# Optimization experiments

Hardware: AMD Instinct MI355X
Metric: run time of the kernel (lower is better)

Reference implementation:

```python
import jax, jax.numpy as jnp
import numpy as np

D_STATE = 8
D_CONV = 4
DT_RANK = 8
THRESHOLD = 0.5
KPOOL = 3
PAD = (KPOOL - 1) // 2
EPS = 1e-5


def _rmsnorm(x, w):
    return x * jax.lax.rsqrt(jnp.mean(x * x, axis=-1, keepdims=True) + EPS) * w


def _dw_causal_conv(x, w, b):
    # x: (L, T, C), w: (C, 1, K) depthwise causal conv along T
    xt = jnp.transpose(x, (0, 2, 1))  # (L, C, T)
    y = jax.lax.conv_general_dilated(
        xt, w, window_strides=(1,), padding=[(D_CONV - 1, 0)],
        dimension_numbers=('NCH', 'OIH', 'NCH'), feature_group_count=xt.shape[1])
    return jnp.transpose(y, (0, 2, 1)) + b


def _selective_scan(x, delta, A, B, Cm, D):
    # x, delta: (L,T,d); A: (d,n); B, Cm: (L,T,n); D: (d,)
    dA = jnp.exp(delta[..., None] * A)                        # (L,T,d,n)
    dBx = (delta * x)[..., None] * B[:, :, None, :]           # (L,T,d,n)
    def combine(a, b):
        a1, b1 = a
        a2, b2 = b
        return (a2 * a1, a2 * b1 + b2)
    _, h = jax.lax.associative_scan(combine, (dA, dBx), axis=1)
    y = jnp.einsum('ltdn,ltn->ltd', h, Cm)
    return y + x * D


def _mamba_block(x, in_proj, conv_w, conv_b, x_proj_w, dt_proj_w, dt_proj_b,
                 A_log_f, A_log_b, D_f, D_b, out_proj_w, rms_w):
    # single-depth bidirectional (bimamba-v2 style) block, expand=1, residual + RMSNorm
    res = x
    xn = _rmsnorm(x, rms_w)
    xz = xn @ in_proj                       # (L,T,2C)
    xi, z = jnp.split(xz, 2, axis=-1)
    xi = jax.nn.silu(_dw_causal_conv(xi, conv_w, conv_b))
    dbl = xi @ x_proj_w                     # (L,T,dt_rank+2*d_state)
    dt = dbl[..., :DT_RANK]
    Bm = dbl[..., DT_RANK:DT_RANK + D_STATE]
    Cm = dbl[..., DT_RANK + D_STATE:]
    delta = jax.nn.softplus(dt @ dt_proj_w + dt_proj_b)
    A_f = -jnp.exp(A_log_f)
    A_b = -jnp.exp(A_log_b)
    flip = lambda a: a[:, ::-1]
    y_f = _selective_scan(xi, delta, A_f, Bm, Cm, D_f)
    y_b = flip(_selective_scan(flip(xi), flip(delta), A_b, flip(Bm), flip(Cm), D_b))
    y = 0.5 * (y_f + y_b) * jax.nn.silu(z)  # if_devide_out -> average two directions
    return res + y @ out_proj_w


def reference(feats, in_proj, conv_w, conv_b, x_proj_w, dt_proj_w, dt_proj_b,
              A_log_f, A_log_b, D_f, D_b, out_proj_w, rms_w, mlp_w, mlp_b,
              record_len):
    N, C, H, W = feats.shape
    T = H * W
    rec = np.asarray(record_len)  # static ragged group sizes
    ends = np.cumsum(rec)
    starts = ends - rec
    masks = []
    for s0, L in zip(starts.tolist(), rec.tolist()):
        g = feats[s0:s0 + L]                       # (L,C,H,W)
        if L > 1:
            x = g.reshape(L, C, T).transpose(0, 2, 1)  # l c h w -> l (h w) c
            feat = _mamba_block(x, in_proj, conv_w, conv_b, x_proj_w, dt_proj_w,
                                dt_proj_b, A_log_f, A_log_b, D_f, D_b,
                                out_proj_w, rms_w)
            score = jax.nn.sigmoid(feat @ mlp_w + mlp_b)   # (L,T,1)
            ego = jnp.ones((1, T, 1), feats.dtype)
            bs = jnp.concatenate([ego, score[1:]], axis=0)
        else:
            bs = jnp.ones((1, T, 1), feats.dtype)
        bs = bs.transpose(0, 2, 1).reshape(L, 1, H, W)     # l (h w) c -> l c h w
        masks.append(jnp.where(bs > THRESHOLD, 1.0, 0.0).astype(feats.dtype))
    mask = jnp.concatenate(masks, axis=0)                  # (N,1,H,W)
    pooled = jax.lax.reduce_window(
        mask, -jnp.inf, jax.lax.max,
        window_dimensions=(1, 1, KPOOL, KPOOL), window_strides=(1, 1, 1, 1),
        padding=[(0, 0), (0, 0), (PAD, PAD), (PAD, PAD)])
    return pooled


def setup_inputs():
    key = jax.random.key(0)
    ks = jax.random.split(key, 8)
    C, H, W = 128, 96, 96
    record_len = np.array([2, 3, 1, 2, 4], dtype=np.int64)
    N = int(record_len.sum())
    s = 0.05
    A_log = jnp.log(jnp.broadcast_to(
        jnp.arange(1, D_STATE + 1, dtype=jnp.float32), (C, D_STATE)))
    return {
        'feats': jax.random.normal(ks[0], (N, C, H, W), jnp.float32),
        'in_proj': jax.random.normal(ks[1], (C, 2 * C), jnp.float32) * s,
        'conv_w': jax.random.normal(ks[2], (C, 1, D_CONV), jnp.float32) * s,
        'conv_b': jnp.zeros((C,), jnp.float32),
        'x_proj_w': jax.random.normal(ks[3], (C, DT_RANK + 2 * D_STATE), jnp.float32) * s,
        'dt_proj_w': jax.random.normal(ks[4], (DT_RANK, C), jnp.float32) * s,
        'dt_proj_b': jnp.full((C,), 0.1, jnp.float32),
        'A_log_f': A_log,
        'A_log_b': A_log,
        'D_f': jnp.ones((C,), jnp.float32),
        'D_b': jnp.ones((C,), jnp.float32),
        'out_proj_w': jax.random.normal(ks[5], (C, C), jnp.float32) * s,
        'rms_w': jnp.ones((C,), jnp.float32),
        'mlp_w': jax.random.normal(ks[6], (C, 1), jnp.float32) * s,
        'mlp_b': jnp.zeros((1,), jnp.float32),
        'record_len': jnp.asarray(record_len),
    }
```

## Files before the change

### kernel.cpp

```cpp
#include <hip/hip_runtime.h>
#include <cstdint>
#include <cstddef>

#define C_CH 128
#define T_TOK 9216
#define H_IMG 96
#define W_IMG 96
#define NSTATE 8

#define CHUNK 64
#define RHALO 32

#define MT 128
#define NT 128
#define KS 32

__device__ __forceinline__ float siluf_dev(float x) {
  return x / (1.0f + expf(-x));
}

__global__ __launch_bounds__(256) void k0_setup(
    const int* __restrict__ rec, int n_groups, int N,
    const float* __restrict__ out_proj_w, const float* __restrict__ mlp_w,
    const float* __restrict__ in_proj, const float* __restrict__ rms_w,
    float* __restrict__ vvec, int* __restrict__ slot, float* __restrict__ Bf)
{
  const int tid = threadIdx.x;
  if (tid == 0) {
    int f = 0, sl = 0;
    for (int g = 0; g < n_groups; ++g) {
      const int L = rec[g];
      slot[f] = -1;
      for (int i = 1; i < L; ++i) slot[f + i] = sl++;
      f += L;
    }
  }
  if (tid < C_CH) {
    float acc = 0.0f;
    for (int j = 0; j < C_CH; ++j) acc += out_proj_w[tid * C_CH + j] * mlp_w[j];
    vvec[tid] = acc;
  }
  for (int idx = tid; idx < C_CH * 256; idx += 256) {
    const int k = idx >> 8;
    Bf[idx] = in_proj[idx] * rms_w[k];
  }
}

__global__ __launch_bounds__(256, 4) void k1_gemm(
    const float* __restrict__ feats, const float* __restrict__ Bf,
    const float* __restrict__ mlp_w, const float* __restrict__ mlp_b,
    const float* __restrict__ vvec, const int* __restrict__ slot,
    float* __restrict__ xipre, float* __restrict__ wbuf,
    float* __restrict__ logit)
{
  __shared__ float Asm[KS * MT];
  __shared__ float Bsm[KS * NT];
  __shared__ float redS[256], redR[256], irS[MT];
  const int f = blockIdx.z;
  const int s = slot[f];
  if (s < 0) return;
  const int m0 = blockIdx.x * MT;
  const int nch = blockIdx.y;
  const int j0 = nch * NT;
  const int tid = threadIdx.x;
  const int tm = tid & 15;
  const int tn = tid >> 4;
  const size_t fbase = (size_t)f * C_CH * T_TOK;
  const size_t rowbase = (size_t)s * T_TOK;

  float acc[8][8];
  #pragma unroll
  for (int i = 0; i < 8; ++i)
    #pragma unroll
    for (int j = 0; j < 8; ++j) acc[i][j] = 0.0f;
  float ssum = 0.0f, rmsum = 0.0f;
  const int tokA = tid & 127;
  const int khalf = tid >> 7;

  for (int ks = 0; ks < 4; ++ks) {
    const int k0 = ks * KS;
    __syncthreads();
    #pragma unroll
    for (int i = 0; i < 4; ++i) {
      const int idx = tid + 256 * i;
      const int r = idx >> 5;
      const int q = (idx & 31) * 4;
      *(float4*)&Asm[r * MT + q] =
          *(const float4*)&feats[fbase + (size_t)(k0 + r) * T_TOK + m0 + q];
      *(float4*)&Bsm[r * NT + q] =
          *(const float4*)&Bf[(k0 + r) * 256 + j0 + q];
    }
    __syncthreads();
    #pragma unroll
    for (int kk = 0; kk < 16; ++kk) {
      const int k = khalf * 16 + kk;
      const float v = Asm[k * MT + tokA];
      ssum = fmaf(v, v, ssum);
      rmsum = fmaf(v, mlp_w[k0 + k], rmsum);
    }
    #pragma unroll 8
    for (int k = 0; k < KS; ++k) {
      const float4 a0 = *(const float4*)&Asm[k * MT + tm * 8];
      const float4 a1 = *(const float4*)&Asm[k * MT + tm * 8 + 4];
      const float4 b0 = *(const float4*)&Bsm[k * NT + tn * 8];
      const float4 b1 = *(const float4*)&Bsm[k * NT + tn * 8 + 4];
      const float ar[8] = {a0.x, a0.y, a0.z, a0.w, a1.x, a1.y, a1.z, a1.w};
      const float br[8] = {b0.x, b0.y, b0.z, b0.w, b1.x, b1.y, b1.z, b1.w};
      #pragma unroll
      for (int i = 0; i < 8; ++i)
        #pragma unroll
        for (int j = 0; j < 8; ++j)
          acc[i][j] = fmaf(ar[i], br[j], acc[i][j]);
    }
  }
  redS[tid] = ssum; redR[tid] = rmsum;
  __syncthreads();
  if (tid < 128) {
    const float ss = redS[tid] + redS[tid + 128];
    irS[tid] = 1.0f / sqrtf(ss * (1.0f / C_CH) + 1e-5f);
    if (nch == 0)
      logit[rowbase + m0 + tid] = redR[tid] + redR[tid + 128] + mlp_b[0];
  }
  __syncthreads();

  if (nch == 0) {
    #pragma unroll
    for (int i = 0; i < 8; ++i) {
      const int t = m0 + tm * 8 + i;
      const float irv = irS[tm * 8 + i];
      float4 o0, o1;
      o0.x = acc[i][0] * irv; o0.y = acc[i][1] * irv;
      o0.z = acc[i][2] * irv; o0.w = acc[i][3] * irv;
      o1.x = acc[i][4] * irv; o1.y = acc[i][5] * irv;
      o1.z = acc[i][6] * irv; o1.w = acc[i][7] * irv;
      float* dst = &xipre[(rowbase + t) * C_CH + tn * 8];
      *(float4*)dst = o0;
      *(float4*)(dst + 4) = o1;
    }
  } else {
    const float4 v0 = *(const float4*)&vvec[tn * 8];
    const float4 v1 = *(const float4*)&vvec[tn * 8 + 4];
    const float vr[8] = {v0.x, v0.y, v0.z, v0.w, v1.x, v1.y, v1.z, v1.w};
    #pragma unroll
    for (int i = 0; i < 8; ++i) {
      const int t = m0 + tm * 8 + i;
      const float irv = irS[tm * 8 + i];
      float o[8];
      #pragma unroll
      for (int j = 0; j < 8; ++j) {
        const float z = acc[i][j] * irv;
        o[j] = 0.5f * (z / (1.0f + __expf(-z))) * vr[j];
      }
      float* dst = &wbuf[(rowbase + t) * C_CH + tn * 8];
      *(float4*)dst = *(float4*)&o[0];
      *(float4*)(dst + 4) = *(float4*)&o[4];
    }
  }
}

__global__ __launch_bounds__(256, 5) void k3_fused(
    const float* __restrict__ xipre, const float* __restrict__ wbuf,
    const float* __restrict__ conv_w, const float* __restrict__ conv_b,
    const float* __restrict__ x_proj_w,
    const float* __restrict__ dt_proj_w, const float* __restrict__ dt_proj_b,
    const float* __restrict__ A_log_f, const float* __restrict__ A_log_b,
    const float* __restrict__ D_f, const float* __restrict__ D_b,
    const int* __restrict__ slot, float* __restrict__ logit)
{
  __shared__ float xibuf[32 * 129];
  __shared__ float dbl[128 * 24];
  const int f = blockIdx.y;
  const int s = slot[f];
  if (s < 0) return;
  const int c0 = blockIdx.x * CHUNK;
  const int r0 = c0 - RHALO;
  const int tid = threadIdx.x;
  const int c = tid & 127;
  const int half = tid >> 7;
  const size_t rowbase = (size_t)s * T_TOK;
  const float4 cw = *(const float4*)(conv_w + c * 4);
  const float cb = conv_b[c];

  auto ldx = [&](int t) -> float {
    return (t >= 0 && t < T_TOK) ? xipre[(rowbase + t) * C_CH + c] : 0.0f;
  };

  const int q6 = __builtin_amdgcn_readfirstlane(tid >> 6) * 6;
  const int tok = tid & 63;
  for (int pass = 0; pass < 4; ++pass) {
    __syncthreads();
    {
      const int pr0 = pass * 32 + half * 16;
      float xm1 = ldx(r0 + pr0 - 1);
      float xm2 = ldx(r0 + pr0 - 2);
      float xm3 = ldx(r0 + pr0 - 3);
      for (int i = 0; i < 16; ++i) {
        const float cur = ldx(r0 + pr0 + i);
        const float sum = cw.x * xm3 + cw.y * xm2 + cw.z * xm1 + cw.w * cur + cb;
        xibuf[(half * 16 + i) * 129 + c] = sum / (1.0f + __expf(-sum));
        xm3 = xm2; xm2 = xm1; xm1 = cur;
      }
    }
    __syncthreads();
    if (tok < 32) {
      float acc[6] = {0, 0, 0, 0, 0, 0};
      for (int cc = 0; cc < C_CH; ++cc) {
        const float xv = xibuf[tok * 129 + cc];
        #pragma unroll
        for (int jj = 0; jj < 6; ++jj)
          acc[jj] += xv * x_proj_w[cc * 24 + q6 + jj];
      }
      #pragma unroll
      for (int jj = 0; jj < 6; ++jj)
        dbl[(pass * 32 + tok) * 24 + q6 + jj] = acc[jj];
    }
  }
  __syncthreads();

  float dw[8], Ac[8];
  const float* Alog = half ? A_log_b : A_log_f;
  #pragma unroll
  for (int r = 0; r < 8; ++r) dw[r] = dt_proj_w[r * C_CH + c];
  #pragma unroll
  for (int n = 0; n < NSTATE; ++n) Ac[n] = -expf(Alog[c * NSTATE + n]);
  bool fa = true;
  #pragma unroll
  for (int n = 0; n < NSTATE; ++n)
    fa = fa && (fabsf(Ac[n] - (n + 1) * Ac[0]) < 1e-5f * (n + 1));
  const bool fast = (__ballot(fa) == 0xFFFFFFFFFFFFFFFFull);
  const float bias = dt_proj_b[c];
  const float Dd = half ? D_b[c] : D_f[c];
  float h[8] = {0, 0, 0, 0, 0, 0, 0, 0};

  if (half == 0) {
    const int tb = (r0 < 0) ? 0 : r0;
    const int steps = c0 + CHUNK - tb;
    const int outg0 = (c0 - tb) >> 3;
    const int ng = steps >> 3;
    float xm1 = ldx(tb - 1), xm2 = ldx(tb - 2), xm3 = ldx(tb - 3);
    for (int g = 0; g < ng; ++g) {
      const int t0 = tb + g * 8;
      const bool out = (g >= outg0);
      float pg[8], wg[8];
      #pragma unroll
      for (int j = 0; j < 8; ++j) {
        const size_t gi = (rowbase + t0 + j) * C_CH + c;
        pg[j] = xipre[gi];
        wg[j] = out ? wbuf[gi] : 0.0f;
      }
      #pragma unroll
      for (int j = 0; j < 8; ++j) {
        const int t = t0 + j;
        const int p = t - r0;
        const float cur = pg[j];
        const float sum = cw.x * xm3 + cw.y * xm2 + cw.z * xm1 + cw.w * cur + cb;
        const float xiv = sum / (1.0f + __expf(-sum));
        xm3 = xm2; xm2 = xm1; xm1 = cur;
        const float4 d0 = *(const float4*)&dbl[p * 24];
        const float4 d1 = *(const float4*)&dbl[p * 24 + 4];
        float pre = bias;
        pre += d0.x * dw[0] + d0.y * dw[1] + d0.z * dw[2] + d0.w * dw[3];
        pre += d1.x * dw[4] + d1.y * dw[5] + d1.z * dw[6] + d1.w * dw[7];
        const float dlt = fmaxf(pre, 0.0f) + __logf(1.0f + __expf(-fabsf(pre)));
        const float u = dlt * xiv;
        float e[8];
        if (fast) {
          const float r1 = __expf(dlt * Ac[0]);
          e[0] = r1; e[1] = r1 * r1; e[2] = e[1] * r1; e[3] = e[2] * r1;
          e[4] = e[3] * r1; e[5] = e[4] * r1; e[6] = e[5] * r1; e[7] = e[6] * r1;
        } else {
          #pragma unroll
          for (int n = 0; n < 8; ++n) e[n] = __expf(dlt * Ac[n]);
        }
        const float4 b0 = *(const float4*)&dbl[p * 24 + 8];
        const float4 b1 = *(const float4*)&dbl[p * 24 + 12];
        h[0] = e[0] * h[0] + u * b0.x; h[1] = e[1] * h[1] + u * b0.y;
        h[2] = e[2] * h[2] + u * b0.z; h[3] = e[3] * h[3] + u * b0.w;
        h[4] = e[4] * h[4] + u * b1.x; h[5] = e[5] * h[5] + u * b1.y;
        h[6] = e[6] * h[6] + u * b1.z; h[7] = e[7] * h[7] + u * b1.w;
        if (out) {
          const float4 cc0 = *(const float4*)&dbl[p * 24 + 16];
          const float4 cc1 = *(const float4*)&dbl[p * 24 + 20];
          float y = xiv * Dd;
          y += h[0] * cc0.x + h[1] * cc0.y + h[2] * cc0.z + h[3] * cc0.w;
          y += h[4] * cc1.x + h[5] * cc1.y + h[6] * cc1.z + h[7] * cc1.w;
          float contrib = y * wg[j];
          contrib += __shfl_xor(contrib, 1);
          contrib += __shfl_xor(contrib, 2);
          contrib += __shfl_xor(contrib, 4);
          contrib += __shfl_xor(contrib, 8);
          contrib += __shfl_xor(contrib, 16);
          contrib += __shfl_xor(contrib, 32);
          if ((tid & 63) == 0) atomicAdd(&logit[rowbase + t], contrib);
        }
      }
    }
  } else {
    const int te2e = r0 + 128;
    const int te2 = (te2e > T_TOK) ? T_TOK : te2e;
    const int steps = te2 - c0;
    const int outg0 = (te2 - (c0 + CHUNK)) >> 3;
    const int ng = steps >> 3;
    float w0 = ldx(te2 - 1), w1 = ldx(te2 - 2), w2 = ldx(te2 - 3), w3 = ldx(te2 - 4);
    for (int g = 0; g < ng; ++g) {
      const int t0 = te2 - 1 - g * 8;
      const bool out = (g >= outg0);
      float nv[8], wg[8];
      #pragma unroll
      for (int j = 0; j < 8; ++j) {
        nv[j] = ldx(t0 - 4 - j);
        wg[j] = out ? wbuf[(rowbase + t0 - j) * C_CH + c] : 0.0f;
      }
      #pragma unroll
      for (int j = 0; j < 8; ++j) {
        const int t = t0 - j;
        const int p = t - r0;
        const float sum = cw.x * w3 + cw.y * w2 + cw.z * w1 + cw.w * w0 + cb;
        const float xiv = sum / (1.0f + __expf(-sum));
        w0 = w1; w1 = w2; w2 = w3; w3 = nv[j];
        const float4 d0 = *(const float4*)&dbl[p * 24];
        const float4 d1 = *(const float4*)&dbl[p * 24 + 4];
        float pre = bias;
        pre += d0.x * dw[0] + d0.y * dw[1] + d0.z * dw[2] + d0.w * dw[3];
        pre += d1.x * dw[4] + d1.y * dw[5] + d1.z * dw[6] + d1.w * dw[7];
        const float dlt = fmaxf(pre, 0.0f) + __logf(1.0f + __expf(-fabsf(pre)));
        const float u = dlt * xiv;
        float e[8];
        if (fast) {
          const float r1 = __expf(dlt * Ac[0]);
          e[0] = r1; e[1] = r1 * r1; e[2] = e[1] * r1; e[3] = e[2] * r1;
          e[4] = e[3] * r1; e[5] = e[4] * r1; e[6] = e[5] * r1; e[7] = e[6] * r1;
        } else {
          #pragma unroll
          for (int n = 0; n < 8; ++n) e[n] = __expf(dlt * Ac[n]);
        }
        const float4 b0 = *(const float4*)&dbl[p * 24 + 8];
        const float4 b1 = *(const float4*)&dbl[p * 24 + 12];
        h[0] = e[0] * h[0] + u * b0.x; h[1] = e[1] * h[1] + u * b0.y;
        h[2] = e[2] * h[2] + u * b0.z; h[3] = e[3] * h[3] + u * b0.w;
        h[4] = e[4] * h[4] + u * b1.x; h[5] = e[5] * h[5] + u * b1.y;
        h[6] = e[6] * h[6] + u * b1.z; h[7] = e[7] * h[7] + u * b1.w;
        if (out) {
          const float4 cc0 = *(const float4*)&dbl[p * 24 + 16];
          const float4 cc1 = *(const float4*)&dbl[p * 24 + 20];
          float y = xiv * Dd;
          y += h[0] * cc0.x + h[1] * cc0.y + h[2] * cc0.z + h[3] * cc0.w;
          y += h[4] * cc1.x + h[5] * cc1.y + h[6] * cc1.z + h[7] * cc1.w;
          float contrib = y * wg[j];
          contrib += __shfl_xor(contrib, 1);
          contrib += __shfl_xor(contrib, 2);
          contrib += __shfl_xor(contrib, 4);
          contrib += __shfl_xor(contrib, 8);
          contrib += __shfl_xor(contrib, 16);
          contrib += __shfl_xor(contrib, 32);
          if ((tid & 63) == 0) atomicAdd(&logit[rowbase + t], contrib);
        }
      }
    }
  }
}

__global__ __launch_bounds__(128) void k4_pool(
    const float* __restrict__ logit, const int* __restrict__ slot,
    float* __restrict__ out)
{
  const int w = threadIdx.x;
  if (w >= W_IMG) return;
  const int hh = blockIdx.x;
  const int f = blockIdx.y;
  const int s = slot[f];
  float m = 0.0f;
  if (s < 0) {
    m = 1.0f;
  } else {
    for (int dh = -1; dh <= 1; ++dh) {
      const int h2 = hh + dh;
      if (h2 < 0 || h2 >= H_IMG) continue;
      for (int dw = -1; dw <= 1; ++dw) {
        const int w2 = w + dw;
        if (w2 < 0 || w2 >= W_IMG) continue;
        if (logit[(size_t)s * T_TOK + h2 * W_IMG + w2] > 0.0f) m = 1.0f;
      }
    }
  }
  out[(size_t)f * T_TOK + hh * W_IMG + w] = m;
}

extern "C" void kernel_launch(void* const* d_in, const int* in_sizes, int n_in,
                              void* d_out, int out_size, void* d_ws, size_t ws_size,
                              hipStream_t stream) {
  const float* feats      = (const float*)d_in[0];
  const float* in_proj    = (const float*)d_in[1];
  const float* conv_w     = (const float*)d_in[2];
  const float* conv_b     = (const float*)d_in[3];
  const float* x_proj_w   = (const float*)d_in[4];
  const float* dt_proj_w  = (const float*)d_in[5];
  const float* dt_proj_b  = (const float*)d_in[6];
  const float* A_log_f    = (const float*)d_in[7];
  const float* A_log_b    = (const float*)d_in[8];
  const float* D_f        = (const float*)d_in[9];
  const float* D_b        = (const float*)d_in[10];
  const float* out_proj_w = (const float*)d_in[11];
  const float* rms_w      = (const float*)d_in[12];
  const float* mlp_w      = (const float*)d_in[13];
  const float* mlp_b      = (const float*)d_in[14];
  const int*   rec        = (const int*)d_in[15];

  const int N = in_sizes[0] / (C_CH * T_TOK);
  const int n_groups = in_sizes[15];
  int S = N - n_groups;
  if (S < 1) S = 1;

  char* p = (char*)d_ws;
  float* vvec  = (float*)p; p += 1024;
  int*   slot  = (int*)p;   p += ((N * 4 + 255) / 256) * 256;
  float* Bf    = (float*)p; p += C_CH * 256 * 4;
  float* logit = (float*)p; p += (size_t)S * T_TOK * 4;
  float* xipre = (float*)p; p += (size_t)S * T_TOK * C_CH * 4;
  float* wA    = (float*)p; p += (size_t)S * T_TOK * C_CH * 4;
  (void)ws_size; (void)n_in; (void)out_size;

  k0_setup<<<1, 256, 0, stream>>>(rec, n_groups, N, out_proj_w, mlp_w,
                                  in_proj, rms_w, vvec, slot, Bf);
  k1_gemm<<<dim3(T_TOK / MT, 2, N), 256, 0, stream>>>(
      feats, Bf, mlp_w, mlp_b, vvec, slot, xipre, wA, logit);
  k3_fused<<<dim3(T_TOK / CHUNK, N), 256, 0, stream>>>(
      xipre, wA, conv_w, conv_b, x_proj_w, dt_proj_w, dt_proj_b,
      A_log_f, A_log_b, D_f, D_b, slot, logit);
  k4_pool<<<dim3(H_IMG, N), 128, 0, stream>>>(logit, slot, (float*)d_out);
}
```

Measured before the change: 372.1 us.

## Prefetch GEMM and scan inputs into registers, reduce logits in shared memory

The GEMM kernel now register-prefetches the next K-slab of feats and weights while computing on the current one. The scan kernel double-buffers its per-group global loads of xipre and wbuf. The four per-wave atomicAdds per token are replaced by a shared-memory partial buffer and a single non-atomic add per token at the end of the block. It also swaps divisions for hardware reciprocal, shortens the power chain for the exponentials, and lowers occupancy hints and the unroll factor. The extra registers from prefetching trade against occupancy, and the non-atomic logit update relies on each block exclusively owning its token range.

Result: slower. 419.1 us (+12.7%).

```diff
diff --git a/kernel.cpp b/kernel.cpp
--- a/kernel.cpp
+++ b/kernel.cpp
@@ -17,6 +17,9 @@
 
 __device__ __forceinline__ float siluf_dev(float x) {
   return x / (1.0f + expf(-x));
+}
+__device__ __forceinline__ float fast_rcp(float x) {
+  return __builtin_amdgcn_rcpf(x);
 }
 
 __global__ __launch_bounds__(256) void k0_setup(
@@ -46,7 +49,7 @@
   }
 }
 
-__global__ __launch_bounds__(256, 4) void k1_gemm(
+__global__ __launch_bounds__(256, 3) void k1_gemm(
     const float* __restrict__ feats, const float* __restrict__ Bf,
     const float* __restrict__ mlp_w, const float* __restrict__ mlp_b,
     const float* __restrict__ vvec, const int* __restrict__ slot,
@@ -77,6 +80,16 @@
   const int tokA = tid & 127;
   const int khalf = tid >> 7;
 
+  float4 pa[4], pb[4];
+  #pragma unroll
+  for (int i = 0; i < 4; ++i) {
+    const int idx = tid + 256 * i;
+    const int r = idx >> 5;
+    const int q = (idx & 31) * 4;
+    pa[i] = *(const float4*)&feats[fbase + (size_t)r * T_TOK + m0 + q];
+    pb[i] = *(const float4*)&Bf[r * 256 + j0 + q];
+  }
+
   for (int ks = 0; ks < 4; ++ks) {
     const int k0 = ks * KS;
     __syncthreads();
@@ -85,12 +98,20 @@
       const int idx = tid + 256 * i;
       const int r = idx >> 5;
       const int q = (idx & 31) * 4;
-      *(float4*)&Asm[r * MT + q] =
-          *(const float4*)&feats[fbase + (size_t)(k0 + r) * T_TOK + m0 + q];
-      *(float4*)&Bsm[r * NT + q] =
-          *(const float4*)&Bf[(k0 + r) * 256 + j0 + q];
+      *(float4*)&Asm[r * MT + q] = pa[i];
+      *(float4*)&Bsm[r * NT + q] = pb[i];
     }
     __syncthreads();
+    if (ks < 3) {
+      #pragma unroll
+      for (int i = 0; i < 4; ++i) {
+        const int idx = tid + 256 * i;
+        const int r = (idx >> 5) + k0 + KS;
+        const int q = (idx & 31) * 4;
+        pa[i] = *(const float4*)&feats[fbase + (size_t)r * T_TOK + m0 + q];
+        pb[i] = *(const float4*)&Bf[r * 256 + j0 + q];
+      }
+    }
     #pragma unroll
     for (int kk = 0; kk < 16; ++kk) {
       const int k = khalf * 16 + kk;
@@ -98,7 +119,7 @@
       ssum = fmaf(v, v, ssum);
       rmsum = fmaf(v, mlp_w[k0 + k], rmsum);
     }
-    #pragma unroll 8
+    #pragma unroll 2
     for (int k = 0; k < KS; ++k) {
       const float4 a0 = *(const float4*)&Asm[k * MT + tm * 8];
       const float4 a1 = *(const float4*)&Asm[k * MT + tm * 8 + 4];
@@ -149,7 +170,7 @@
       #pragma unroll
       for (int j = 0; j < 8; ++j) {
         const float z = acc[i][j] * irv;
-        o[j] = 0.5f * (z / (1.0f + __expf(-z))) * vr[j];
+        o[j] = 0.5f * z * fast_rcp(1.0f + __expf(-z)) * vr[j];
       }
       float* dst = &wbuf[(rowbase + t) * C_CH + tn * 8];
       *(float4*)dst = *(float4*)&o[0];
@@ -158,7 +179,7 @@
   }
 }
 
-__global__ __launch_bounds__(256, 5) void k3_fused(
+__global__ __launch_bounds__(256, 4) void k3_fused(
     const float* __restrict__ xipre, const float* __restrict__ wbuf,
     const float* __restrict__ conv_w, const float* __restrict__ conv_b,
     const float* __restrict__ x_proj_w,
@@ -169,6 +190,7 @@
 {
   __shared__ float xibuf[32 * 129];
   __shared__ float dbl[128 * 24];
+  __shared__ float part[4][64];
   const int f = blockIdx.y;
   const int s = slot[f];
   if (s < 0) return;
@@ -177,6 +199,7 @@
   const int tid = threadIdx.x;
   const int c = tid & 127;
   const int half = tid >> 7;
+  const int wv = tid >> 6;
   const size_t rowbase = (size_t)s * T_TOK;
   const float4 cw = *(const float4*)(conv_w + c * 4);
   const float cb = conv_b[c];
@@ -197,7 +220,7 @@
       for (int i = 0; i < 16; ++i) {
         const float cur = ldx(r0 + pr0 + i);
         const float sum = cw.x * xm3 + cw.y * xm2 + cw.z * xm1 + cw.w * cur + cb;
-        xibuf[(half * 16 + i) * 129 + c] = sum / (1.0f + __expf(-sum));
+        xibuf[(half * 16 + i) * 129 + c] = sum * fast_rcp(1.0f + __expf(-sum));
         xm3 = xm2; xm2 = xm1; xm1 = cur;
       }
     }
@@ -230,6 +253,7 @@
   const bool fast = (__ballot(fa) == 0xFFFFFFFFFFFFFFFFull);
   const float bias = dt_proj_b[c];
   const float Dd = half ? D_b[c] : D_f[c];
+  const float Ac0 = Ac[0];
   float h[8] = {0, 0, 0, 0, 0, 0, 0, 0};
 
   if (half == 0) {
@@ -238,23 +262,36 @@
     const int outg0 = (c0 - tb) >> 3;
     const int ng = steps >> 3;
     float xm1 = ldx(tb - 1), xm2 = ldx(tb - 2), xm3 = ldx(tb - 3);
+    float pgA[8], wgA[8];
+    {
+      const bool o0 = (0 >= outg0);
+      #pragma unroll
+      for (int j = 0; j < 8; ++j) {
+        const size_t gi = (rowbase + tb + j) * C_CH + c;
+        pgA[j] = xipre[gi];
+        wgA[j] = o0 ? wbuf[gi] : 0.0f;
+      }
+    }
     for (int g = 0; g < ng; ++g) {
       const int t0 = tb + g * 8;
       const bool out = (g >= outg0);
-      float pg[8], wg[8];
-      #pragma unroll
-      for (int j = 0; j < 8; ++j) {
-        const size_t gi = (rowbase + t0 + j) * C_CH + c;
-        pg[j] = xipre[gi];
-        wg[j] = out ? wbuf[gi] : 0.0f;
+      float pgB[8], wgB[8];
+      if (g + 1 < ng) {
+        const bool oN = (g + 1 >= outg0);
+        #pragma unroll
+        for (int j = 0; j < 8; ++j) {
+          const size_t gi = (rowbase + t0 + 8 + j) * C_CH + c;
+          pgB[j] = xipre[gi];
+          wgB[j] = oN ? wbuf[gi] : 0.0f;
+        }
       }
       #pragma unroll
       for (int j = 0; j < 8; ++j) {
         const int t = t0 + j;
         const int p = t - r0;
-        const float cur = pg[j];
+        const float cur = pgA[j];
         const float sum = cw.x * xm3 + cw.y * xm2 + cw.z * xm1 + cw.w * cur + cb;
-        const float xiv = sum / (1.0f + __expf(-sum));
+        const float xiv = sum * fast_rcp(1.0f + __expf(-sum));
         xm3 = xm2; xm2 = xm1; xm1 = cur;
         const float4 d0 = *(const float4*)&dbl[p * 24];
         const float4 d1 = *(const float4*)&dbl[p * 24 + 4];
@@ -265,9 +302,10 @@
         const float u = dlt * xiv;
         float e[8];
         if (fast) {
-          const float r1 = __expf(dlt * Ac[0]);
-          e[0] = r1; e[1] = r1 * r1; e[2] = e[1] * r1; e[3] = e[2] * r1;
-          e[4] = e[3] * r1; e[5] = e[4] * r1; e[6] = e[5] * r1; e[7] = e[6] * r1;
+          const float r1 = __expf(dlt * Ac0);
+          const float r2 = r1 * r1, r4 = r2 * r2;
+          e[0] = r1; e[1] = r2; e[2] = r2 * r1; e[3] = r4;
+          e[4] = r4 * r1; e[5] = r4 * r2; e[6] = r4 * e[2]; e[7] = r4 * r4;
         } else {
           #pragma unroll
           for (int n = 0; n < 8; ++n) e[n] = __expf(dlt * Ac[n]);
@@ -284,15 +322,19 @@
           float y = xiv * Dd;
           y += h[0] * cc0.x + h[1] * cc0.y + h[2] * cc0.z + h[3] * cc0.w;
           y += h[4] * cc1.x + h[5] * cc1.y + h[6] * cc1.z + h[7] * cc1.w;
-          float contrib = y * wg[j];
+          float contrib = y * wgA[j];
           contrib += __shfl_xor(contrib, 1);
           contrib += __shfl_xor(contrib, 2);
           contrib += __shfl_xor(contrib, 4);
           contrib += __shfl_xor(contrib, 8);
           contrib += __shfl_xor(contrib, 16);
           contrib += __shfl_xor(contrib, 32);
-          if ((tid & 63) == 0) atomicAdd(&logit[rowbase + t], contrib);
-        }
+          if ((tid & 63) == 0) part[wv][t - c0] = contrib;
+        }
+      }
+      if (g + 1 < ng) {
+        #pragma unroll
+        for (int j = 0; j < 8; ++j) { pgA[j] = pgB[j]; wgA[j] = wgB[j]; }
       }
     }
   } else {
@@ -302,22 +344,36 @@
     const int outg0 = (te2 - (c0 + CHUNK)) >> 3;
     const int ng = steps >> 3;
     float w0 = ldx(te2 - 1), w1 = ldx(te2 - 2), w2 = ldx(te2 - 3), w3 = ldx(te2 - 4);
+    float nvA[8], wgA[8];
+    {
+      const bool o0 = (0 >= outg0);
+      const int t0 = te2 - 1;
+      #pragma unroll
+      for (int j = 0; j < 8; ++j) {
+        nvA[j] = ldx(t0 - 4 - j);
+        wgA[j] = o0 ? wbuf[(rowbase + t0 - j) * C_CH + c] : 0.0f;
+      }
+    }
     for (int g = 0; g < ng; ++g) {
       const int t0 = te2 - 1 - g * 8;
       const bool out = (g >= outg0);
-      float nv[8], wg[8];
-      #pragma unroll
-      for (int j = 0; j < 8; ++j) {
-        nv[j] = ldx(t0 - 4 - j);
-        wg[j] = out ? wbuf[(rowbase + t0 - j) * C_CH + c] : 0.0f;
+      float nvB[8], wgB[8];
+      if (g + 1 < ng) {
+        const bool oN = (g + 1 >= outg0);
+        const int t0n = t0 - 8;
+        #pragma unroll
+        for (int j = 0; j < 8; ++j) {
+          nvB[j] = ldx(t0n - 4 - j);
+          wgB[j] = oN ? wbuf[(rowbase + t0n - j) * C_CH + c] : 0.0f;
+        }
       }
       #pragma unroll
       for (int j = 0; j < 8; ++j) {
         const int t = t0 - j;
         const int p = t - r0;
         const float sum = cw.x * w3 + cw.y * w2 + cw.z * w1 + cw.w * w0 + cb;
-        const float xiv = sum / (1.0f + __expf(-sum));
-        w0 = w1; w1 = w2; w2 = w3; w3 = nv[j];
+        const float xiv = sum * fast_rcp(1.0f + __expf(-sum));
+        w0 = w1; w1 = w2; w2 = w3; w3 = nvA[j];
         const float4 d0 = *(const float4*)&dbl[p * 24];
         const float4 d1 = *(const float4*)&dbl[p * 24 + 4];
         float pre = bias;
@@ -327,9 +383,10 @@
         const float u = dlt * xiv;
         float e[8];
         if (fast) {
-          const float r1 = __expf(dlt * Ac[0]);
-          e[0] = r1; e[1] = r1 * r1; e[2] = e[1] * r1; e[3] = e[2] * r1;
-          e[4] = e[3] * r1; e[5] = e[4] * r1; e[6] = e[5] * r1; e[7] = e[6] * r1;
+          const float r1 = __expf(dlt * Ac0);
+          const float r2 = r1 * r1, r4 = r2 * r2;
+          e[0] = r1; e[1] = r2; e[2] = r2 * r1; e[3] = r4;
+          e[4] = r4 * r1; e[5] = r4 * r2; e[6] = r4 * e[2]; e[7] = r4 * r4;
         } else {
           #pragma unroll
           for (int n = 0; n < 8; ++n) e[n] = __expf(dlt * Ac[n]);
@@ -346,17 +403,26 @@
           float y = xiv * Dd;
           y += h[0] * cc0.x + h[1] * cc0.y + h[2] * cc0.z + h[3] * cc0.w;
           y += h[4] * cc1.x + h[5] * cc1.y + h[6] * cc1.z + h[7] * cc1.w;
-          float contrib = y * wg[j];
+          float contrib = y * wgA[j];
           contrib += __shfl_xor(contrib, 1);
           contrib += __shfl_xor(contrib, 2);
           contrib += __shfl_xor(contrib, 4);
           contrib += __shfl_xor(contrib, 8);
           contrib += __shfl_xor(contrib, 16);
           contrib += __shfl_xor(contrib, 32);
-          if ((tid & 63) == 0) atomicAdd(&logit[rowbase + t], contrib);
-        }
-      }
-    }
+          if ((tid & 63) == 0) part[wv][t - c0] = contrib;
+        }
+      }
+      if (g + 1 < ng) {
+        #pragma unroll
+        for (int j = 0; j < 8; ++j) { nvA[j] = nvB[j]; wgA[j] = wgB[j]; }
+      }
+    }
+  }
+  __syncthreads();
+  if (tid < 64) {
+    const float add = part[0][tid] + part[1][tid] + part[2][tid] + part[3][tid];
+    logit[rowbase + c0 + tid] += add;
   }
 }
 
```
